# Kernel tuning notes

Hardware: AMD Instinct MI355X
Metric: run time of the kernel (lower is better)

## Reference

```python
import jax, jax.numpy as jnp
import numpy as np

N_NODES = 10000
N_EDGES = 160000
N_TYPES = 128          # rows in SymbolicEmbeddingsVQ table
N_SYMBOLS = 64
PATTERN_LEN = 8
SYMBOL_DIM = 16
HIDDEN = PATTERN_LEN * SYMBOL_DIM  # mode='concat' -> 128
NUM_RADIAL = 6


def setup_inputs() -> dict:
    key = jax.random.key(0)
    ks = jax.random.split(key, 10)
    x = jax.random.randint(ks[0], (N_NODES,), 0, N_TYPES)
    rbf = jax.random.normal(ks[1], (N_EDGES, NUM_RADIAL), dtype=jnp.float32)
    i = jax.random.randint(ks[2], (N_EDGES,), 0, N_NODES)
    j = jax.random.randint(ks[3], (N_EDGES,), 0, N_NODES)
    # VQ symbolic embedding params: each of 128 types is a pattern of
    # PATTERN_LEN symbol ids; symbols are vectors from a codebook.
    code_idx = jax.random.randint(ks[4], (N_TYPES, PATTERN_LEN), 0, N_SYMBOLS)
    codebook = jax.random.normal(ks[5], (N_SYMBOLS, SYMBOL_DIM), dtype=jnp.float32)
    # Linear layers (PyTorch Linear default uniform init approximated by scaled normals)
    W_rbf = jax.random.normal(ks[6], (NUM_RADIAL, HIDDEN), dtype=jnp.float32) / np.sqrt(NUM_RADIAL)
    b_rbf = jnp.zeros((HIDDEN,), dtype=jnp.float32)
    W = jax.random.normal(ks[7], (3 * HIDDEN, HIDDEN), dtype=jnp.float32) / np.sqrt(3 * HIDDEN)
    b = jnp.zeros((HIDDEN,), dtype=jnp.float32)
    return {"x": x, "rbf": rbf, "i": i, "j": j, "code_idx": code_idx,
            "codebook": codebook, "W_rbf": W_rbf, "b_rbf": b_rbf, "W": W, "b": b}


def reference(x, rbf, i, j, code_idx, codebook, W_rbf, b_rbf, W, b):
    act = jax.nn.silu
    # Symbolic VQ embedding, mode='concat': table[t] = concat of PATTERN_LEN codebook vectors
    table = codebook[code_idx].reshape(N_TYPES, HIDDEN)   # [128, hidden]
    h = table[x]                                          # [N_nodes, hidden]
    r = act(rbf @ W_rbf + b_rbf)                          # [E, hidden]
    feat = jnp.concatenate([h[i], h[j], r], axis=-1)      # [E, 3*hidden]
    return act(feat @ W + b)                              # [E, hidden]
```

## Files before the change

kernel.cpp:

```cpp
#include <hip/hip_runtime.h>
#include <hip/hip_bf16.h>
#include <stdint.h>

typedef __attribute__((ext_vector_type(8))) short bf16x8;
typedef __attribute__((ext_vector_type(4))) float f32x4;

__device__ __forceinline__ float silu_f(float x) {
    return x * __builtin_amdgcn_rcpf(1.0f + __expf(-x));
}

__device__ __forceinline__ unsigned short f2bf(float x) {
    union { float f; unsigned int u; } v; v.f = x;
    unsigned int r = v.u + 0x7fffu + ((v.u >> 16) & 1u);
    return (unsigned short)(r >> 16);
}
__device__ __forceinline__ float bf2f(unsigned short u) {
    union { unsigned int u; float f; } v; v.u = ((unsigned int)u) << 16;
    return v.f;
}

__device__ __forceinline__ void async16(void* l, const void* g) {
    auto lds3 = (__attribute__((address_space(3))) unsigned int*)(uintptr_t)l;
    auto g1   = (const __attribute__((address_space(1))) unsigned int*)(uintptr_t)g;
    __builtin_amdgcn_global_load_lds(g1, lds3, 16, 0, 0);
}

__global__ void prep_P(const int* __restrict__ code_idx,
                       const float* __restrict__ codebook,
                       const float* __restrict__ W,
                       const float* __restrict__ b,
                       unsigned short* __restrict__ P1,
                       unsigned short* __restrict__ P2,
                       unsigned short* __restrict__ Wt3)
{
    __shared__ float trow[128];
    const int t = blockIdx.x, tid = threadIdx.x;
    if (tid < 128) {
        int sym = code_idx[t * 8 + (tid >> 4)];
        trow[tid] = codebook[sym * 16 + (tid & 15)];
    } else {
        int k = tid - 128;
        Wt3[t * 128 + k] = f2bf(W[(256 + k) * 128 + t]);
    }
    __syncthreads();
    const int which = tid >> 7, o = tid & 127;
    const float* Wb = W + which * 16384;
    float acc = which ? 0.0f : b[o];
#pragma unroll 8
    for (int k = 0; k < 128; ++k)
        acc += trow[k] * Wb[k * 128 + o];
    (which ? P2 : P1)[t * 128 + o] = f2bf(acc);
}

__global__ __launch_bounds__(256, 3) void fused_main(
    const int* __restrict__ x,
    const float* __restrict__ rbf,
    const int* __restrict__ ei,
    const int* __restrict__ ej,
    const float* __restrict__ W_rbf,
    const float* __restrict__ b_rbf,
    const unsigned short* __restrict__ P1,
    const unsigned short* __restrict__ P2,
    const unsigned short* __restrict__ Wt3,
    float* __restrict__ out)
{
    __shared__ __align__(16) unsigned char lB[32768];
    __shared__ __align__(16) unsigned char lA[16384];
    __shared__ __align__(16) unsigned char lR[1536];

    const int tid  = threadIdx.x;
    const int lane = tid & 63;
    const int w    = tid >> 6;
    const int e0   = blockIdx.x * 64;

    const int quad = lane >> 4, l15 = lane & 15;
    const int wm = (w >> 1) * 32, wn = (w & 1) * 64;

    {
        const int ri = lane >> 4, ch = lane & 15;
#pragma unroll
        for (int rr = 0; rr < 8; ++rr) {
            int g = w * 8 + rr;
            int o = g * 4 + ri;
            int j = ch ^ (o & 7);
            async16(lB + g * 1024, Wt3 + o * 128 + j * 8);
        }
    }
    if (w == 0)
        async16(lR, (const unsigned char*)rbf + (size_t)e0 * 24 + lane * 16);
    else if (w == 1 && lane < 32)
        async16(lR + 1024, (const unsigned char*)rbf + (size_t)e0 * 24 + 1024 + lane * 16);

    int ti[8], tj[8];
#pragma unroll
    for (int mi = 0; mi < 2; ++mi)
#pragma unroll
        for (int r = 0; r < 4; ++r) {
            int m = wm + mi * 16 + quad * 4 + r;
            int e = e0 + m;
            ti[mi * 4 + r] = x[ei[e]];
            tj[mi * 4 + r] = x[ej[e]];
        }

    const int j16 = tid & 15, gg = tid >> 4, cb = j16 * 8;
    float wr[6][8], br[8];
#pragma unroll
    for (int q = 0; q < 6; ++q) {
        const float4* p = (const float4*)(W_rbf + q * 128 + cb);
        float4 a = p[0], c = p[1];
        wr[q][0]=a.x; wr[q][1]=a.y; wr[q][2]=a.z; wr[q][3]=a.w;
        wr[q][4]=c.x; wr[q][5]=c.y; wr[q][6]=c.z; wr[q][7]=c.w;
    }
    {
        const float4* p = (const float4*)(b_rbf + cb);
        float4 a = p[0], c = p[1];
        br[0]=a.x; br[1]=a.y; br[2]=a.z; br[3]=a.w;
        br[4]=c.x; br[5]=c.y; br[6]=c.z; br[7]=c.w;
    }

    __syncthreads();

#pragma unroll
    for (int i = 0; i < 4; ++i) {
        int m = gg * 4 + i;
        const float* rr_ = (const float*)(lR + m * 24);
        float f0 = rr_[0], f1 = rr_[1], f2 = rr_[2],
              f3 = rr_[3], f4 = rr_[4], f5 = rr_[5];
        bf16x8 pk;
#pragma unroll
        for (int c = 0; c < 8; ++c) {
            float a = br[c] + f0*wr[0][c] + f1*wr[1][c] + f2*wr[2][c]
                            + f3*wr[3][c] + f4*wr[4][c] + f5*wr[5][c];
            pk[c] = (short)f2bf(silu_f(a));
        }
        int p = j16 ^ (m & 7);
        *(bf16x8*)(lA + m * 256 + p * 16) = pk;
    }

    __syncthreads();

    unsigned short q1[2][4][4], q2[2][4][4];
#pragma unroll
    for (int mi = 0; mi < 2; ++mi)
#pragma unroll
        for (int r = 0; r < 4; ++r) {
            const unsigned short* p1r = P1 + ti[mi * 4 + r] * 128;
            const unsigned short* p2r = P2 + tj[mi * 4 + r] * 128;
#pragma unroll
            for (int ni = 0; ni < 4; ++ni) {
                int o = wn + ni * 16 + l15;
                q1[mi][r][ni] = p1r[o];
                q2[mi][r][ni] = p2r[o];
            }
        }

    f32x4 acc[2][4] = {};
    const int l7 = l15 & 7;
#pragma unroll
    for (int ks = 0; ks < 4; ++ks) {
        const int j = ks * 4 + quad;
        const int p = j ^ l7;
        bf16x8 af[2], bfv[4];
#pragma unroll
        for (int mi = 0; mi < 2; ++mi)
            af[mi] = *(const bf16x8*)(lA + (wm + mi * 16 + l15) * 256 + p * 16);
#pragma unroll
        for (int ni = 0; ni < 4; ++ni)
            bfv[ni] = *(const bf16x8*)(lB + (wn + ni * 16 + l15) * 256 + p * 16);
#pragma unroll
        for (int mi = 0; mi < 2; ++mi)
#pragma unroll
            for (int ni = 0; ni < 4; ++ni)
                acc[mi][ni] = __builtin_amdgcn_mfma_f32_16x16x32_bf16(
                    af[mi], bfv[ni], acc[mi][ni], 0, 0, 0);
    }

#pragma unroll
    for (int mi = 0; mi < 2; ++mi)
#pragma unroll
        for (int r = 0; r < 4; ++r) {
            int m = wm + mi * 16 + quad * 4 + r;
            size_t e = e0 + m;
#pragma unroll
            for (int ni = 0; ni < 4; ++ni) {
                int o = wn + ni * 16 + l15;
                float v = acc[mi][ni][r] + bf2f(q1[mi][r][ni]) + bf2f(q2[mi][r][ni]);
                out[e * 128 + o] = silu_f(v);
            }
        }
}

extern "C" void kernel_launch(void* const* d_in, const int* in_sizes, int n_in,
                              void* d_out, int out_size, void* d_ws, size_t ws_size,
                              hipStream_t stream) {
    const int*   x        = (const int*)d_in[0];
    const float* rbf      = (const float*)d_in[1];
    const int*   ei       = (const int*)d_in[2];
    const int*   ej       = (const int*)d_in[3];
    const int*   code_idx = (const int*)d_in[4];
    const float* codebook = (const float*)d_in[5];
    const float* W_rbf    = (const float*)d_in[6];
    const float* b_rbf    = (const float*)d_in[7];
    const float* W        = (const float*)d_in[8];
    const float* b        = (const float*)d_in[9];
    float* out = (float*)d_out;

    const int nE = in_sizes[2];

    if (ws_size < 98304) return;
    unsigned short* P1  = (unsigned short*)d_ws;
    unsigned short* P2  = P1 + 16384;
    unsigned short* Wt3 = P2 + 16384;

    prep_P<<<128, 256, 0, stream>>>(code_idx, codebook, W, b, P1, P2, Wt3);
    fused_main<<<nE / 64, 256, 0, stream>>>(x, rbf, ei, ej, W_rbf, b_rbf,
                                            P1, P2, Wt3, out);
}
```

Measured before the change: 134.4 us.

## Transpose MFMA operands so each lane owns a row and stores float4

Swaps the A and B operands of the MFMA so the accumulator layout gives each lane four consecutive output columns of one edge row. This cuts the per-lane index gathers from eight edges to two, turns the P1/P2 loads into 8-byte vector loads, and turns the output writes into 16-byte nontemporal stores instead of scalar scattered stores. Output writes dominate the traffic, so the change targets store efficiency and fewer load instructions. Nontemporal stores bypass caching, which could matter if the consumer rereads the output soon.

```diff
diff --git a/kernel.cpp b/kernel.cpp
--- a/kernel.cpp
+++ b/kernel.cpp
@@ -4,6 +4,7 @@
 
 typedef __attribute__((ext_vector_type(8))) short bf16x8;
 typedef __attribute__((ext_vector_type(4))) float f32x4;
+typedef __attribute__((ext_vector_type(4))) unsigned short u16x4;
 
 __device__ __forceinline__ float silu_f(float x) {
     return x * __builtin_amdgcn_rcpf(1.0f + __expf(-x));
@@ -91,16 +92,13 @@
     else if (w == 1 && lane < 32)
         async16(lR + 1024, (const unsigned char*)rbf + (size_t)e0 * 24 + 1024 + lane * 16);
 
-    int ti[8], tj[8];
-#pragma unroll
-    for (int mi = 0; mi < 2; ++mi)
-#pragma unroll
-        for (int r = 0; r < 4; ++r) {
-            int m = wm + mi * 16 + quad * 4 + r;
-            int e = e0 + m;
-            ti[mi * 4 + r] = x[ei[e]];
-            tj[mi * 4 + r] = x[ej[e]];
-        }
+    int ti[2], tj[2];
+#pragma unroll
+    for (int mi = 0; mi < 2; ++mi) {
+        int e = e0 + wm + mi * 16 + l15;
+        ti[mi] = x[ei[e]];
+        tj[mi] = x[ej[e]];
+    }
 
     const int j16 = tid & 15, gg = tid >> 4, cb = j16 * 8;
     float wr[6][8], br[8];
@@ -139,20 +137,18 @@
 
     __syncthreads();
 
-    unsigned short q1[2][4][4], q2[2][4][4];
-#pragma unroll
-    for (int mi = 0; mi < 2; ++mi)
-#pragma unroll
-        for (int r = 0; r < 4; ++r) {
-            const unsigned short* p1r = P1 + ti[mi * 4 + r] * 128;
-            const unsigned short* p2r = P2 + tj[mi * 4 + r] * 128;
-#pragma unroll
-            for (int ni = 0; ni < 4; ++ni) {
-                int o = wn + ni * 16 + l15;
-                q1[mi][r][ni] = p1r[o];
-                q2[mi][r][ni] = p2r[o];
-            }
-        }
+    u16x4 q1[2][4], q2[2][4];
+#pragma unroll
+    for (int mi = 0; mi < 2; ++mi) {
+        const unsigned short* p1r = P1 + ti[mi] * 128;
+        const unsigned short* p2r = P2 + tj[mi] * 128;
+#pragma unroll
+        for (int ni = 0; ni < 4; ++ni) {
+            int o = wn + ni * 16 + quad * 4;
+            q1[mi][ni] = *(const u16x4*)(p1r + o);
+            q2[mi][ni] = *(const u16x4*)(p2r + o);
+        }
+    }
 
     f32x4 acc[2][4] = {};
     const int l7 = l15 & 7;
@@ -172,22 +168,23 @@
 #pragma unroll
             for (int ni = 0; ni < 4; ++ni)
                 acc[mi][ni] = __builtin_amdgcn_mfma_f32_16x16x32_bf16(
-                    af[mi], bfv[ni], acc[mi][ni], 0, 0, 0);
-    }
-
-#pragma unroll
-    for (int mi = 0; mi < 2; ++mi)
-#pragma unroll
-        for (int r = 0; r < 4; ++r) {
-            int m = wm + mi * 16 + quad * 4 + r;
-            size_t e = e0 + m;
-#pragma unroll
-            for (int ni = 0; ni < 4; ++ni) {
-                int o = wn + ni * 16 + l15;
-                float v = acc[mi][ni][r] + bf2f(q1[mi][r][ni]) + bf2f(q2[mi][r][ni]);
-                out[e * 128 + o] = silu_f(v);
-            }
-        }
+                    bfv[ni], af[mi], acc[mi][ni], 0, 0, 0);
+    }
+
+#pragma unroll
+    for (int mi = 0; mi < 2; ++mi) {
+        size_t e = (size_t)(e0 + wm + mi * 16 + l15);
+        float* orow = out + e * 128 + wn;
+#pragma unroll
+        for (int ni = 0; ni < 4; ++ni) {
+            f32x4 v;
+#pragma unroll
+            for (int r = 0; r < 4; ++r)
+                v[r] = silu_f(acc[mi][ni][r]
+                              + bf2f(q1[mi][ni][r]) + bf2f(q2[mi][ni][r]));
+            __builtin_nontemporal_store(v, (f32x4*)(orow + ni * 16 + quad * 4));
+        }
+    }
 }
 
 extern "C" void kernel_launch(void* const* d_in, const int* in_sizes, int n_in,
```

Result: slower. 150.1 us (+11.7%).
